# Kernel tuning notes

Hardware: AMD Instinct MI355X
Metric: run time of the kernel (lower is better)

Reference implementation:

```python
import jax, jax.numpy as jnp
import numpy as np

H, W = 256, 256          # detector height/width (pixels)
DELX, DELY = 2.0, 2.0    # detector pixel pitch (mm)
EPS = 1e-8


def _rot(theta, phi, gamma):
    """R = Rz(theta) @ Ry(phi) @ Rx(gamma)."""
    ct, st = jnp.cos(theta), jnp.sin(theta)
    cp, sp = jnp.cos(phi), jnp.sin(phi)
    cg, sg = jnp.cos(gamma), jnp.sin(gamma)
    one = jnp.ones_like(ct); zero = jnp.zeros_like(ct)
    Rz = jnp.stack([jnp.stack([ct, -st, zero]), jnp.stack([st, ct, zero]), jnp.stack([zero, zero, one])])
    Ry = jnp.stack([jnp.stack([cp, zero, sp]), jnp.stack([zero, one, zero]), jnp.stack([-sp, zero, cp])])
    Rx = jnp.stack([jnp.stack([one, zero, zero]), jnp.stack([zero, cg, -sg]), jnp.stack([zero, sg, cg])])
    return Rz @ Ry @ Rx


def _make_xrays(sdr, rotations, translations):
    """Source point (3,) and detector-plane targets (H*W, 3)."""
    R = _rot(rotations[0], rotations[1], rotations[2])
    source = sdr * R[:, 0] + translations      # (3,)
    center = -sdr * R[:, 0] + translations     # detector center, opposite side
    u, v = R[:, 1], R[:, 2]                    # detector in-plane basis (unit)
    t = (jnp.arange(-(H // 2), H // 2, dtype=jnp.float32) + 1.0) * DELX  # (H,)
    s = (jnp.arange(-(W // 2), W // 2, dtype=jnp.float32) + 1.0) * DELY  # (W,)
    # cartesian_prod(t, s) @ [u; v]  ->  t_i * u + s_j * v   (t varies slowest)
    targets = t[:, None, None] * u + s[None, :, None] * v    # (H, W, 3)
    targets = targets.reshape(-1, 3) + center                # (H*W, 3)
    return source, targets


def _raytrace(volume, spacing, source, targets):
    """Siddon ray-tracing: line integral of volume along each source->target ray."""
    nx, ny, nz = volume.shape                       # planes per axis = n + 1
    dims = jnp.array([nx + 1, ny + 1, nz + 1], dtype=jnp.float32)
    sdd = targets - source + EPS                     # (R, 3) ray direction (unnormalized)

    # Entry/exit parametric range [alphamin, alphamax] per ray
    a0 = (0.0 * spacing - source) / sdd              # alpha at first planes
    a1 = ((dims - 1.0) * spacing - source) / sdd     # alpha at last planes
    amin = jnp.max(jnp.minimum(a0, a1), axis=-1, keepdims=True)  # (R, 1)
    amax = jnp.min(jnp.maximum(a0, a1), axis=-1, keepdims=True)  # (R, 1)

    # Alphas at every axis-aligned plane intersection
    ax = (jnp.arange(nx + 1, dtype=jnp.float32) * spacing[0] - source[0]) / sdd[:, 0:1]
    ay = (jnp.arange(ny + 1, dtype=jnp.float32) * spacing[1] - source[1]) / sdd[:, 1:2]
    az = (jnp.arange(nz + 1, dtype=jnp.float32) * spacing[2] - source[2]) / sdd[:, 2:3]
    alphas = jnp.concatenate([ax, ay, az], axis=-1)  # (R, P) with P = nx+ny+nz+3

    # Out-of-range alphas -> amax (amax is itself a kept plane intersection, so the
    # extra trailing segments have zero length; equivalent to the torch NaN trick
    # but NaN-free, so gradients stay clean).
    good = (alphas >= amin) & (alphas <= amax)
    alphas = jnp.where(good, alphas, amax)
    alphas = jnp.sort(alphas, axis=-1)

    amid = 0.5 * (alphas[:, :-1] + alphas[:, 1:])    # (R, P-1) segment midpoints
    step = jnp.diff(alphas, axis=-1)                 # (R, P-1) segment lengths (alpha units)

    # Voxel containing each midpoint (trunc == floor for in-volume points)
    pts = source + amid[..., None] * sdd[:, None, :] # (R, P-1, 3)
    idx = jnp.trunc(pts / spacing).astype(jnp.int32)
    idx = jnp.clip(idx, 0, jnp.array([nx - 1, ny - 1, nz - 1], dtype=jnp.int32))
    vox = volume[idx[..., 0], idx[..., 1], idx[..., 2]]  # (R, P-1)

    drr = jnp.sum(vox * step, axis=-1)               # (R,)
    raylength = jnp.linalg.norm(sdd, axis=-1)        # convert alpha units -> mm
    return drr * raylength


def setup_inputs() -> dict:
    key = jax.random.key(0)
    volume = jax.random.uniform(key, (256, 256, 256), dtype=jnp.float32)  # CT attenuation
    spacing = jnp.ones((3,), dtype=jnp.float32)
    sdr = jnp.asarray(300.0, dtype=jnp.float32)
    rotations = jnp.array([np.pi, 0.0, np.pi / 2], dtype=jnp.float32)     # theta, phi, gamma
    translations = jnp.array([128.0, 128.0, 128.0], dtype=jnp.float32)    # volume center
    return {"volume": volume, "spacing": spacing, "sdr": sdr,
            "rotations": rotations, "translations": translations}


def reference(volume, spacing, sdr, rotations, translations):
    source, targets = _make_xrays(sdr, rotations, translations)
    return _raytrace(volume, spacing, source, targets)  # (H*W,)
```

## Files before the change

### kernel.cpp

```cpp
#include <hip/hip_runtime.h>
#include <math.h>


#define NPLANE 256
constexpr int TPR = 16;

__device__ __forceinline__ float palpha(int i, float sp, float src, float rd) {
    return fmaf((float)i, sp, -src) * rd;
}
__device__ __forceinline__ float palpha_f(float fi, float sp, float nsrc, float rd) {
    return fmaf(fi, sp, nsrc) * rd;
}

__global__ __launch_bounds__(256) void drr_kernel(
    const float* __restrict__ vol,
    const float* __restrict__ spacing,
    const float* __restrict__ sdrp,
    const float* __restrict__ rot,
    const float* __restrict__ trans,
    float* __restrict__ out)
{
    int tid  = threadIdx.x;
    int part = tid >> 4;
    int rlo  = tid & 15;
    int g    = ((int)blockIdx.x * 2731) & 4095;
    int rl   = (g << 4) | rlo;

    float theta = rot[0], phi = rot[1], gam = rot[2];
    float ct = cosf(theta), st = sinf(theta);
    float cp = cosf(phi),   sp_ = sinf(phi);
    float cg = cosf(gam),   sg = sinf(gam);

    float r0x = ct * cp, r0y = st * cp, r0z = -sp_;
    float ux = ct * sp_ * sg - st * cg, uy = st * sp_ * sg + ct * cg, uz = cp * sg;
    float vx = ct * sp_ * cg + st * sg, vy = st * sp_ * cg - ct * sg, vz = cp * cg;

    float cost_u = fabsf(ux) * 65536.f + fabsf(uy) * 256.f + fabsf(uz);
    float cost_v = fabsf(vx) * 65536.f + fabsf(vy) * 256.f + fabsf(vz);
    bool tfast = cost_u < cost_v;
    int ti = tfast ? (rl & 255) : (rl >> 8);
    int si = tfast ? (rl >> 8) : (rl & 255);

    float sdr = sdrp[0];
    float tx = trans[0], ty = trans[1], tz = trans[2];

    float sx = sdr * r0x + tx,  sy = sdr * r0y + ty,  sz = sdr * r0z + tz;
    float cxx = -sdr * r0x + tx, cxy = -sdr * r0y + ty, cxz = -sdr * r0z + tz;

    float tval = (float)(ti - 127) * 2.0f;
    float sval = (float)(si - 127) * 2.0f;

    float gx = tval * ux + sval * vx + cxx;
    float gy = tval * uy + sval * vy + cxy;
    float gz = tval * uz + sval * vz + cxz;

    float sdx = gx - sx + 1e-8f;
    float sdy = gy - sy + 1e-8f;
    float sdz = gz - sz + 1e-8f;

    float spx = spacing[0], spy = spacing[1], spz = spacing[2];
    float rdx = 1.0f / sdx, rdy = 1.0f / sdy, rdz = 1.0f / sdz;

    float a0x = palpha(0, spx, sx, rdx), a1x = palpha(NPLANE, spx, sx, rdx);
    float a0y = palpha(0, spy, sy, rdy), a1y = palpha(NPLANE, spy, sy, rdy);
    float a0z = palpha(0, spz, sz, rdz), a1z = palpha(NPLANE, spz, sz, rdz);

    float amin = fmaxf(fmaxf(fminf(a0x, a1x), fminf(a0y, a1y)), fminf(a0z, a1z));
    float amax = fminf(fminf(fmaxf(a0x, a1x), fmaxf(a0y, a1y)), fmaxf(a0z, a1z));

    float acc = 0.f;

    if (amax > amin) {
        float range = amax - amin;
        constexpr float inv = 1.0f / (float)TPR;
        float lo = fmaf(range, (float)part * inv, amin);
        float hi = (part == TPR - 1) ? INFINITY
                                     : fmaf(range, (float)(part + 1) * inv, amin);
        float end = fminf(hi, amax);

        int ix, iy, iz, dix, diy, diz;
        float nxx, nxy, nxz;

        #define SETUP(SP, SRC, SDD, RD, I, DI, NXT)                                \
        {                                                                          \
            float q = fmaf(lo, SDD, SRC) / (SP);                                   \
            q = fminf(fmaxf(q, -1.f), 257.f);                                      \
            if ((SDD) > 0.f) {                                                     \
                DI = 1;                                                            \
                I = (int)ceilf(q);                                                 \
                while (I > 0 && palpha(I - 1, SP, SRC, RD) >= lo) --I;             \
                while (I <= NPLANE && palpha(I, SP, SRC, RD) < lo) ++I;            \
                NXT = (I <= NPLANE) ? palpha(I, SP, SRC, RD) : INFINITY;           \
            } else {                                                               \
                DI = -1;                                                           \
                I = (int)floorf(q);                                                \
                while (I < NPLANE && palpha(I + 1, SP, SRC, RD) >= lo) ++I;        \
                while (I >= 0 && palpha(I, SP, SRC, RD) < lo) --I;                 \
                NXT = (I >= 0) ? palpha(I, SP, SRC, RD) : INFINITY;                \
            }                                                                      \
        }

        SETUP(spx, sx, sdx, rdx, ix, dix, nxx)
        SETUP(spy, sy, sdy, rdy, iy, diy, nxy)
        SETUP(spz, sz, sdz, rdz, iz, diz, nxz)
        #undef SETUP

        float ispy = 1.0f / spy, ispz = 1.0f / spz;
        float sdyE = sdy * ispy, syE = sy * ispy;
        float sdzE = sdz * ispz, szE = sz * ispz;

        float fiy = (float)iy, fiz = (float)iz;
        float dfy = (float)diy, dfz = (float)diz;
        float nsy = -sy, nsz = -sz;
        int offcx = (dix > 0) ? -1 : 0;

        #define ADV()                                                              \
            if (nxx == cur) { ix += dix; nxx = palpha(ix, spx, sx, rdx); }         \
            if (nxy == cur) { fiy += dfy; nxy = palpha_f(fiy, spy, nsy, rdy); }    \
            if (nxz == cur) { fiz += dfz; nxz = palpha_f(fiz, spz, nsz, rdz); }

        #define SEG_ADDR(CUR, E, ADDR)                                             \
        {                                                                          \
            float amid = 0.5f * ((CUR) + (E));                                     \
            float pyv = fmaf(amid, sdyE, syE);                                     \
            float pzv = fmaf(amid, sdzE, szE);                                     \
            int jx = ix + offcx; jx = jx < 0 ? 0 : (jx > 255 ? 255 : jx);          \
            int jy = (int)pyv;   jy = jy < 0 ? 0 : (jy > 255 ? 255 : jy);          \
            int jz = (int)pzv;   jz = jz < 0 ? 0 : (jz > 255 ? 255 : jz);          \
            ADDR = (jx << 16) + (jy << 8) + jz;                                    \
        }

        float cur = fminf(fminf(nxx, nxy), nxz);

        if (cur < end) {
            ADV();
            float nxt = fminf(fminf(nxx, nxy), nxz);
            float e   = fminf(nxt, amax);
            int addr; SEG_ADDR(cur, e, addr)
            float pstep = e - cur;
            float pval  = vol[addr];
            cur = nxt;

            while (cur < end) {
                ADV();
                nxt = fminf(fminf(nxx, nxy), nxz);
                e   = fminf(nxt, amax);
                int addr2; SEG_ADDR(cur, e, addr2)
                float nval = vol[addr2];
                acc = fmaf(pval, pstep, acc);
                pval  = nval;
                pstep = e - cur;
                cur = nxt;
            }
            acc = fmaf(pval, pstep, acc);
        }
        #undef ADV
        #undef SEG_ADDR
    }

    acc += __shfl_xor(acc, 16);
    acc += __shfl_xor(acc, 32);

    __shared__ float red[64];
    int wave = tid >> 6;
    if ((tid & 63) < 16)
        red[(wave << 4) | rlo] = acc;
    __syncthreads();

    if (tid < 16) {
        float s = red[tid] + red[16 + tid] + red[32 + tid] + red[48 + tid];
        float rl2 = sqrtf(sdx * sdx + sdy * sdy + sdz * sdz);
        out[ti * 256 + si] = s * rl2;
    }
}

extern "C" void kernel_launch(void* const* d_in, const int* in_sizes, int n_in,
                              void* d_out, int out_size, void* d_ws, size_t ws_size,
                              hipStream_t stream) {
    const float* vol     = (const float*)d_in[0];
    const float* spacing = (const float*)d_in[1];
    const float* sdr     = (const float*)d_in[2];
    const float* rot     = (const float*)d_in[3];
    const float* trans   = (const float*)d_in[4];
    float* out = (float*)d_out;

    int nblocks = 256 * 256 / 16;
    drr_kernel<<<nblocks, 256, 0, stream>>>(vol, spacing, sdr, rot, trans, out);
}
```

Measured before the change: 63.18 us.

## Precompute per-ray setup in a separate kernel and read records from workspace

Moves rotation, ray direction, reciprocal and entry/exit parameter computation into a new ray_setup kernel that writes 64-byte per-ray records to workspace. The main traversal kernel loads these records instead of recomputing trig and setup in all 16 threads per ray. It also removes the block index scrambling, so blocks are processed in linear ray order. The cost is an extra kernel launch, extra global memory traffic, and a possible change in load balance from dropping the permutation.

After: 69.39 us. +9.8%, slower.

```diff
diff --git a/kernel.cpp b/kernel.cpp
--- a/kernel.cpp
+++ b/kernel.cpp
@@ -12,61 +12,89 @@
     return fmaf(fi, sp, nsrc) * rd;
 }
 
-__global__ __launch_bounds__(256) void drr_kernel(
-    const float* __restrict__ vol,
+__global__ __launch_bounds__(256) void ray_setup(
     const float* __restrict__ spacing,
     const float* __restrict__ sdrp,
     const float* __restrict__ rot,
     const float* __restrict__ trans,
+    float* __restrict__ ws)
+{
+    int rl = (int)blockIdx.x * 256 + threadIdx.x;
+
+    float theta = rot[0], phi = rot[1], gam = rot[2];
+    float ct = cosf(theta), st = sinf(theta);
+    float cp = cosf(phi),   sp_ = sinf(phi);
+    float cg = cosf(gam),   sg = sinf(gam);
+
+    float r0x = ct * cp, r0y = st * cp, r0z = -sp_;
+    float ux = ct*sp_*sg - st*cg, uy = st*sp_*sg + ct*cg, uz = cp*sg;
+    float vx = ct*sp_*cg + st*sg, vy = st*sp_*cg - ct*sg, vz = cp*cg;
+
+    float cost_u = fabsf(ux)*65536.f + fabsf(uy)*256.f + fabsf(uz);
+    float cost_v = fabsf(vx)*65536.f + fabsf(vy)*256.f + fabsf(vz);
+    bool tfast = cost_u < cost_v;
+    int ti = tfast ? (rl & 255) : (rl >> 8);
+    int si = tfast ? (rl >> 8) : (rl & 255);
+
+    float sdr = sdrp[0];
+    float tx = trans[0], ty = trans[1], tz = trans[2];
+
+    float sx = sdr*r0x + tx,  sy = sdr*r0y + ty,  sz = sdr*r0z + tz;
+    float cxx = -sdr*r0x + tx, cxy = -sdr*r0y + ty, cxz = -sdr*r0z + tz;
+
+    float tval = (float)(ti - 127) * 2.0f;
+    float sval = (float)(si - 127) * 2.0f;
+
+    float gx = tval*ux + sval*vx + cxx;
+    float gy = tval*uy + sval*vy + cxy;
+    float gz = tval*uz + sval*vz + cxz;
+
+    float sdx = gx - sx + 1e-8f;
+    float sdy = gy - sy + 1e-8f;
+    float sdz = gz - sz + 1e-8f;
+
+    float spx = spacing[0], spy = spacing[1], spz = spacing[2];
+    float rdx = 1.f/sdx, rdy = 1.f/sdy, rdz = 1.f/sdz;
+
+    float a0x = palpha(0,spx,sx,rdx), a1x = palpha(NPLANE,spx,sx,rdx);
+    float a0y = palpha(0,spy,sy,rdy), a1y = palpha(NPLANE,spy,sy,rdy);
+    float a0z = palpha(0,spz,sz,rdz), a1z = palpha(NPLANE,spz,sz,rdz);
+
+    float amin = fmaxf(fmaxf(fminf(a0x,a1x), fminf(a0y,a1y)), fminf(a0z,a1z));
+    float amax = fminf(fminf(fmaxf(a0x,a1x), fmaxf(a0y,a1y)), fmaxf(a0z,a1z));
+
+    float rlen = sqrtf(sdx*sdx + sdy*sdy + sdz*sdz);
+    float ispy = 1.f/spy, ispz = 1.f/spz;
+
+    float4* rec = (float4*)(ws + (size_t)rl * 16);
+    rec[0] = make_float4(sx, sy, sz, sdx);
+    rec[1] = make_float4(sdy, sdz, rdx, rdy);
+    rec[2] = make_float4(rdz, amin, amax, rlen);
+    rec[3] = make_float4(sdy*ispy, sy*ispy, sdz*ispz, sz*ispz);
+
+    if (rl == 0)
+        *(int*)(ws + (size_t)65536 * 16) = tfast ? 1 : 0;
+}
+
+__global__ __launch_bounds__(256) void drr_kernel(
+    const float* __restrict__ vol,
+    const float* __restrict__ spacing,
+    const float* __restrict__ ws,
     float* __restrict__ out)
 {
     int tid  = threadIdx.x;
     int part = tid >> 4;
     int rlo  = tid & 15;
-    int g    = ((int)blockIdx.x * 2731) & 4095;
-    int rl   = (g << 4) | rlo;
-
-    float theta = rot[0], phi = rot[1], gam = rot[2];
-    float ct = cosf(theta), st = sinf(theta);
-    float cp = cosf(phi),   sp_ = sinf(phi);
-    float cg = cosf(gam),   sg = sinf(gam);
-
-    float r0x = ct * cp, r0y = st * cp, r0z = -sp_;
-    float ux = ct * sp_ * sg - st * cg, uy = st * sp_ * sg + ct * cg, uz = cp * sg;
-    float vx = ct * sp_ * cg + st * sg, vy = st * sp_ * cg - ct * sg, vz = cp * cg;
-
-    float cost_u = fabsf(ux) * 65536.f + fabsf(uy) * 256.f + fabsf(uz);
-    float cost_v = fabsf(vx) * 65536.f + fabsf(vy) * 256.f + fabsf(vz);
-    bool tfast = cost_u < cost_v;
-    int ti = tfast ? (rl & 255) : (rl >> 8);
-    int si = tfast ? (rl >> 8) : (rl & 255);
-
-    float sdr = sdrp[0];
-    float tx = trans[0], ty = trans[1], tz = trans[2];
-
-    float sx = sdr * r0x + tx,  sy = sdr * r0y + ty,  sz = sdr * r0z + tz;
-    float cxx = -sdr * r0x + tx, cxy = -sdr * r0y + ty, cxz = -sdr * r0z + tz;
-
-    float tval = (float)(ti - 127) * 2.0f;
-    float sval = (float)(si - 127) * 2.0f;
-
-    float gx = tval * ux + sval * vx + cxx;
-    float gy = tval * uy + sval * vy + cxy;
-    float gz = tval * uz + sval * vz + cxz;
-
-    float sdx = gx - sx + 1e-8f;
-    float sdy = gy - sy + 1e-8f;
-    float sdz = gz - sz + 1e-8f;
+    int rl   = ((int)blockIdx.x << 4) | rlo;
+
+    const float4* rec = (const float4*)(ws + (size_t)rl * 16);
+    float4 q0 = rec[0], q1 = rec[1], q2 = rec[2], q3 = rec[3];
+    float sx = q0.x,  sy = q0.y,  sz = q0.z,  sdx = q0.w;
+    float sdy = q1.x, sdz = q1.y, rdx = q1.z, rdy = q1.w;
+    float rdz = q2.x, amin = q2.y, amax = q2.z, rlen = q2.w;
+    float sdyE = q3.x, syE = q3.y, sdzE = q3.z, szE = q3.w;
 
     float spx = spacing[0], spy = spacing[1], spz = spacing[2];
-    float rdx = 1.0f / sdx, rdy = 1.0f / sdy, rdz = 1.0f / sdz;
-
-    float a0x = palpha(0, spx, sx, rdx), a1x = palpha(NPLANE, spx, sx, rdx);
-    float a0y = palpha(0, spy, sy, rdy), a1y = palpha(NPLANE, spy, sy, rdy);
-    float a0z = palpha(0, spz, sz, rdz), a1z = palpha(NPLANE, spz, sz, rdz);
-
-    float amin = fmaxf(fmaxf(fminf(a0x, a1x), fminf(a0y, a1y)), fminf(a0z, a1z));
-    float amax = fminf(fminf(fmaxf(a0x, a1x), fmaxf(a0y, a1y)), fmaxf(a0z, a1z));
 
     float acc = 0.f;
 
@@ -105,10 +133,6 @@
         SETUP(spz, sz, sdz, rdz, iz, diz, nxz)
         #undef SETUP
 
-        float ispy = 1.0f / spy, ispz = 1.0f / spz;
-        float sdyE = sdy * ispy, syE = sy * ispy;
-        float sdzE = sdz * ispz, szE = sz * ispz;
-
         float fiy = (float)iy, fiz = (float)iz;
         float dfy = (float)diy, dfz = (float)diz;
         float nsy = -sy, nsz = -sz;
@@ -169,8 +193,10 @@
 
     if (tid < 16) {
         float s = red[tid] + red[16 + tid] + red[32 + tid] + red[48 + tid];
-        float rl2 = sqrtf(sdx * sdx + sdy * sdy + sdz * sdz);
-        out[ti * 256 + si] = s * rl2;
+        int tfast = *(const int*)(ws + (size_t)65536 * 16);
+        int ti = tfast ? (rl & 255) : (rl >> 8);
+        int si = tfast ? (rl >> 8) : (rl & 255);
+        out[ti * 256 + si] = s * rlen;
     }
 }
 
@@ -183,7 +209,10 @@
     const float* rot     = (const float*)d_in[3];
     const float* trans   = (const float*)d_in[4];
     float* out = (float*)d_out;
+    float* ws  = (float*)d_ws;
+
+    ray_setup<<<256, 256, 0, stream>>>(spacing, sdr, rot, trans, ws);
 
     int nblocks = 256 * 256 / 16;
-    drr_kernel<<<nblocks, 256, 0, stream>>>(vol, spacing, sdr, rot, trans, out);
-}
+    drr_kernel<<<nblocks, 256, 0, stream>>>(vol, spacing, ws, out);
+}
```
